# Kernel tuning notes

Hardware: AMD Instinct MI355X
Metric: run time of the kernel (lower is better)

Reference implementation:

```python
import jax, jax.numpy as jnp
import numpy as np

N_E = 8192
E_DIM = 256
BETA = 0.25
SIGMA = 0.1


def setup_inputs() -> dict:
    key = jax.random.key(0)
    kz, ke = jax.random.split(key)
    z = jax.random.normal(kz, (16, 256, 32, 32), dtype=jnp.float32)
    # torch init: uniform(-1/n_e, 1/n_e)
    emb = jax.random.uniform(ke, (N_E, E_DIM), minval=-1.0 / N_E, maxval=1.0 / N_E, dtype=jnp.float32)
    return {"z": z, "emb": emb}


def _vq_forward(z, emb, beta=BETA, sigma=SIGMA):
    b, c, h, w = z.shape  # c == e_dim
    z_bhwc = jnp.transpose(z, (0, 2, 3, 1))  # b h w c
    zf = z_bhwc.reshape(-1, c)  # [b*h*w, c]

    # d[i, n] = ||zf_i||^2 + ||e_n||^2 - 2 zf_i . e_n
    e2 = jnp.sum(emb ** 2, axis=1)  # [n_e]
    d = jnp.sum(zf ** 2, axis=1, keepdims=True) + e2 - 2.0 * (zf @ emb.T)  # [bhw, n_e]

    # codebook-codebook pairwise distances
    d1 = e2[:, None] + e2[None, :] - 2.0 * (emb @ emb.T)  # [n_e, n_e]
    # torch.kthvalue(d1, 2, 0): 2nd smallest along dim 0, per column
    min_dist = jnp.sort(d1, axis=0)[1]  # [n_e]
    total_min_distance = jnp.sum(min_dist)
    codebookvariance = jnp.std(min_dist, ddof=1)  # torch.std is unbiased

    min_encoding_indices = jnp.argmin(d, axis=1)  # [bhw]
    # d[range, argmin] == row-wise min
    distances = jnp.min(d, axis=1).reshape(b, h, w)
    # rbf: exp(-(d^2).mean(axis=1) / (2*sigma^2)) -> [b, w]
    distances = jnp.exp(-jnp.mean(distances ** 2, axis=1) / (2.0 * sigma ** 2))

    z_q = jnp.take(emb, min_encoding_indices, axis=0).reshape(b, h, w, c)

    sg = jax.lax.stop_gradient
    # legacy=True branch
    loss = (jnp.mean((sg(z_q) - z_bhwc) ** 2)
            + beta * jnp.mean((z_q - sg(z_bhwc)) ** 2)
            - total_min_distance)

    # straight-through estimator
    z_q = z_bhwc + sg(z_q - z_bhwc)
    z_q_bchw = jnp.transpose(z_q, (0, 3, 1, 2))  # b c h w (contiguous)
    # torch .view(b, h*w, e_dim) on contiguous bchw buffer: raw reshape
    z_flattened1 = z_q_bchw.reshape(b, h * w, c)

    return (z_q_bchw, loss, distances, min_encoding_indices,
            z_flattened1, codebookvariance, total_min_distance)


def reference(z, emb):
    return _vq_forward(z, emb)
```

## Files before the change

kernel.cpp:

```cpp
#include <hip/hip_runtime.h>
#include <stdint.h>

#define N_E   8192
#define EDIM  256
#define NB    16
#define HH    32
#define WW    32
#define HW    1024
#define NI    16384
#define NELEM 4194304

#define O_ZQ   0
#define O_LOSS 4194304
#define O_DIST 4194305
#define O_IDX  4194817
#define O_ZFL  4211201
#define O_CBV  8405505
#define O_TMD  8405506

#define WS_PMIN 0
#define WS_IDX  131072
#define WS_DMIN 196608
#define WS_E2   262144
#define WS_Z2   294912
#define WS_MSE  360448
#define WS_D1P  360512

__device__ __forceinline__ int row8(int ty, int r) {
    return (r < 4) ? (ty * 4 + r) : (64 + ty * 4 + (r - 4));
}

__global__ void k_init(unsigned long long* __restrict__ pmin, double* __restrict__ mse) {
    int t = blockIdx.x * 256 + threadIdx.x;
    if (t < NI) pmin[t] = 0xFFFFFFFFFFFFFFFFull;
    if (t == 0) *mse = 0.0;
}

__global__ void k_e2(const float* __restrict__ emb, float* __restrict__ e2) {
    int row  = blockIdx.x * 4 + (threadIdx.x >> 6);
    int lane = threadIdx.x & 63;
    float4 v = *reinterpret_cast<const float4*>(emb + (size_t)row * EDIM + lane * 4);
    float s = v.x * v.x + v.y * v.y + v.z * v.z + v.w * v.w;
    #pragma unroll
    for (int m = 32; m; m >>= 1) s += __shfl_xor(s, m);
    if (lane == 0) e2[row] = s;
}

__global__ void k_z2(const float* __restrict__ z, float* __restrict__ z2) {
    int i = blockIdx.x * 256 + threadIdx.x;
    int b = i >> 10, hw = i & 1023;
    const float* p = z + (size_t)b * EDIM * HW + hw;
    float s = 0.f;
    #pragma unroll 8
    for (int c = 0; c < EDIM; ++c) { float v = p[(size_t)c * HW]; s += v * v; }
    z2[i] = s;
}

__launch_bounds__(256)
__global__ void k_gemm_z(const float* __restrict__ z, const float* __restrict__ emb,
                         const float* __restrict__ z2, const float* __restrict__ e2,
                         unsigned long long* __restrict__ pmin) {
    __shared__ float a_lds[16][128];
    __shared__ float b_lds[16][128];
    const int t  = threadIdx.x;
    const int tx = t & 15, ty = t >> 4;
    const int i0 = blockIdx.x * 128;
    const int bb = i0 >> 10, hw0 = i0 & 1023;
    const int nbase = blockIdx.y * 1024;

    float minv[8], z2r[8];
    int   mini[8];
    #pragma unroll
    for (int r = 0; r < 8; ++r) {
        minv[r] = 3.4e38f; mini[r] = 0x7fffffff;
        z2r[r]  = z2[i0 + row8(ty, r)];
    }

    const int ak = t >> 4;
    const int ax = (t & 15) * 4;
    const float* zbase = z + (size_t)bb * EDIM * HW + hw0;
    const int bj = t >> 1;
    const int bc = (t & 1) * 8;

    for (int ns = 0; ns < 8; ++ns) {
        const int n0 = nbase + ns * 128;
        float acc[8][8];
        #pragma unroll
        for (int r = 0; r < 8; ++r)
            #pragma unroll
            for (int c = 0; c < 8; ++c) acc[r][c] = 0.f;

        for (int kc = 0; kc < 16; ++kc) {
            const int c0 = kc * 16;
            __syncthreads();
            *reinterpret_cast<float4*>(&a_lds[ak][ax]) =
                *reinterpret_cast<const float4*>(zbase + (size_t)(c0 + ak) * HW + ax);
            *reinterpret_cast<float4*>(&a_lds[ak][ax + 64]) =
                *reinterpret_cast<const float4*>(zbase + (size_t)(c0 + ak) * HW + ax + 64);
            {
                const float4 u = *reinterpret_cast<const float4*>(emb + (size_t)(n0 + bj) * EDIM + c0 + bc);
                const float4 v = *reinterpret_cast<const float4*>(emb + (size_t)(n0 + bj) * EDIM + c0 + bc + 4);
                b_lds[bc + 0][bj] = u.x; b_lds[bc + 1][bj] = u.y;
                b_lds[bc + 2][bj] = u.z; b_lds[bc + 3][bj] = u.w;
                b_lds[bc + 4][bj] = v.x; b_lds[bc + 5][bj] = v.y;
                b_lds[bc + 6][bj] = v.z; b_lds[bc + 7][bj] = v.w;
            }
            __syncthreads();
            #pragma unroll
            for (int k = 0; k < 16; ++k) {
                const float4 a0 = *reinterpret_cast<const float4*>(&a_lds[k][ty * 4]);
                const float4 a1 = *reinterpret_cast<const float4*>(&a_lds[k][64 + ty * 4]);
                const float4 b0 = *reinterpret_cast<const float4*>(&b_lds[k][tx * 4]);
                const float4 b1 = *reinterpret_cast<const float4*>(&b_lds[k][64 + tx * 4]);
                const float av[8] = {a0.x, a0.y, a0.z, a0.w, a1.x, a1.y, a1.z, a1.w};
                const float bv[8] = {b0.x, b0.y, b0.z, b0.w, b1.x, b1.y, b1.z, b1.w};
                #pragma unroll
                for (int r = 0; r < 8; ++r)
                    #pragma unroll
                    for (int c = 0; c < 8; ++c)
                        acc[r][c] = fmaf(av[r], bv[c], acc[r][c]);
            }
        }
        const float4 e0 = *reinterpret_cast<const float4*>(&e2[n0 + tx * 4]);
        const float4 e1 = *reinterpret_cast<const float4*>(&e2[n0 + 64 + tx * 4]);
        const float ev[8] = {e0.x, e0.y, e0.z, e0.w, e1.x, e1.y, e1.z, e1.w};
        #pragma unroll
        for (int r = 0; r < 8; ++r) {
            #pragma unroll
            for (int c = 0; c < 8; ++c) {
                const float d = (z2r[r] + ev[c]) - 2.0f * acc[r][c];
                const int   n = n0 + ((c < 4) ? (tx * 4 + c) : (64 + tx * 4 + (c - 4)));
                if (d < minv[r]) { minv[r] = d; mini[r] = n; }
            }
        }
    }
    #pragma unroll
    for (int r = 0; r < 8; ++r) {
        #pragma unroll
        for (int m = 1; m < 16; m <<= 1) {
            const float ov = __shfl_xor(minv[r], m);
            const int   oi = __shfl_xor(mini[r], m);
            if (ov < minv[r] || (ov == minv[r] && oi < mini[r])) { minv[r] = ov; mini[r] = oi; }
        }
        if (tx == 0) {
            const unsigned long long pk =
                ((unsigned long long)__float_as_uint(minv[r]) << 32) | (unsigned)mini[r];
            atomicMin(&pmin[i0 + row8(ty, r)], pk);
        }
    }
}

__launch_bounds__(256)
__global__ void k_gemm_d1(const float* __restrict__ emb, const float* __restrict__ e2,
                          float* __restrict__ d1p) {
    __shared__ float a_lds[16][128];
    __shared__ float b_lds[16][128];
    const int t  = threadIdx.x;
    const int tx = t & 15, ty = t >> 4;
    const int n0A   = blockIdx.x * 128;
    const int mbase = blockIdx.y * 1024;

    float v1[8], v2[8], e2a[8];
    #pragma unroll
    for (int r = 0; r < 8; ++r) { v1[r] = 3.4e38f; v2[r] = 3.4e38f; e2a[r] = e2[n0A + row8(ty, r)]; }

    const int aj = t >> 1;
    const int ac = (t & 1) * 8;

    for (int ms = 0; ms < 8; ++ms) {
        const int m0 = mbase + ms * 128;
        float acc[8][8];
        #pragma unroll
        for (int r = 0; r < 8; ++r)
            #pragma unroll
            for (int c = 0; c < 8; ++c) acc[r][c] = 0.f;

        for (int kc = 0; kc < 16; ++kc) {
            const int c0 = kc * 16;
            __syncthreads();
            {
                const float4 u = *reinterpret_cast<const float4*>(emb + (size_t)(n0A + aj) * EDIM + c0 + ac);
                const float4 v = *reinterpret_cast<const float4*>(emb + (size_t)(n0A + aj) * EDIM + c0 + ac + 4);
                a_lds[ac + 0][aj] = u.x; a_lds[ac + 1][aj] = u.y;
                a_lds[ac + 2][aj] = u.z; a_lds[ac + 3][aj] = u.w;
                a_lds[ac + 4][aj] = v.x; a_lds[ac + 5][aj] = v.y;
                a_lds[ac + 6][aj] = v.z; a_lds[ac + 7][aj] = v.w;
            }
            {
                const float4 u = *reinterpret_cast<const float4*>(emb + (size_t)(m0 + aj) * EDIM + c0 + ac);
                const float4 v = *reinterpret_cast<const float4*>(emb + (size_t)(m0 + aj) * EDIM + c0 + ac + 4);
                b_lds[ac + 0][aj] = u.x; b_lds[ac + 1][aj] = u.y;
                b_lds[ac + 2][aj] = u.z; b_lds[ac + 3][aj] = u.w;
                b_lds[ac + 4][aj] = v.x; b_lds[ac + 5][aj] = v.y;
                b_lds[ac + 6][aj] = v.z; b_lds[ac + 7][aj] = v.w;
            }
            __syncthreads();
            #pragma unroll
            for (int k = 0; k < 16; ++k) {
                const float4 a0 = *reinterpret_cast<const float4*>(&a_lds[k][ty * 4]);
                const float4 a1 = *reinterpret_cast<const float4*>(&a_lds[k][64 + ty * 4]);
                const float4 b0 = *reinterpret_cast<const float4*>(&b_lds[k][tx * 4]);
                const float4 b1 = *reinterpret_cast<const float4*>(&b_lds[k][64 + tx * 4]);
                const float av[8] = {a0.x, a0.y, a0.z, a0.w, a1.x, a1.y, a1.z, a1.w};
                const float bv[8] = {b0.x, b0.y, b0.z, b0.w, b1.x, b1.y, b1.z, b1.w};
                #pragma unroll
                for (int r = 0; r < 8; ++r)
                    #pragma unroll
                    for (int c = 0; c < 8; ++c)
                        acc[r][c] = fmaf(av[r], bv[c], acc[r][c]);
            }
        }
        const float4 e0 = *reinterpret_cast<const float4*>(&e2[m0 + tx * 4]);
        const float4 e1 = *reinterpret_cast<const float4*>(&e2[m0 + 64 + tx * 4]);
        const float eb[8] = {e0.x, e0.y, e0.z, e0.w, e1.x, e1.y, e1.z, e1.w};
        #pragma unroll
        for (int r = 0; r < 8; ++r) {
            #pragma unroll
            for (int c = 0; c < 8; ++c) {
                const float d = (eb[c] + e2a[r]) - 2.0f * acc[r][c];
                if (d < v1[r]) { v2[r] = v1[r]; v1[r] = d; }
                else if (d < v2[r]) { v2[r] = d; }
            }
        }
    }
    #pragma unroll
    for (int r = 0; r < 8; ++r) {
        #pragma unroll
        for (int m = 1; m < 16; m <<= 1) {
            const float o1 = __shfl_xor(v1[r], m);
            const float o2 = __shfl_xor(v2[r], m);
            const float nv1 = fminf(v1[r], o1);
            const float nv2 = fminf(fmaxf(v1[r], o1), fminf(v2[r], o2));
            v1[r] = nv1; v2[r] = nv2;
        }
        if (tx == 0) {
            const int n = n0A + row8(ty, r);
            d1p[((size_t)blockIdx.y * N_E + n) * 2 + 0] = v1[r];
            d1p[((size_t)blockIdx.y * N_E + n) * 2 + 1] = v2[r];
        }
    }
}

__global__ void k_unpack(const unsigned long long* __restrict__ pmin,
                         int* __restrict__ idxi, float* __restrict__ dmin,
                         float* __restrict__ out_idx) {
    int i = blockIdx.x * 256 + threadIdx.x;
    unsigned long long p = pmin[i];
    int idx  = (int)(p & 0xFFFFFFFFull);
    idxi[i]  = idx;
    dmin[i]  = __uint_as_float((unsigned)(p >> 32));
    out_idx[i] = (float)idx;
}

__global__ void k_epilogue(const float* __restrict__ z, const float* __restrict__ emb,
                           const int* __restrict__ idxi,
                           float* __restrict__ out_zq, float* __restrict__ out_zfl,
                           double* __restrict__ mse) {
    const int j4 = blockIdx.x * 256 + threadIdx.x;
    const int j  = j4 * 4;
    const int b  = j >> 18;
    const int c  = (j >> 10) & 255;
    const int hw = j & 1023;
    const int ib = (b << 10) + hw;
    const float4 zv = *reinterpret_cast<const float4*>(z + j);
    const float q0 = emb[(size_t)idxi[ib + 0] * EDIM + c];
    const float q1 = emb[(size_t)idxi[ib + 1] * EDIM + c];
    const float q2 = emb[(size_t)idxi[ib + 2] * EDIM + c];
    const float q3 = emb[(size_t)idxi[ib + 3] * EDIM + c];
    const float d0 = q0 - zv.x, d1 = q1 - zv.y, d2 = q2 - zv.z, d3 = q3 - zv.w;
    const float4 st = {zv.x + d0, zv.y + d1, zv.z + d2, zv.w + d3};
    *reinterpret_cast<float4*>(out_zq + j) = st;
    out_zfl[j + 0] = st.x; out_zfl[j + 1] = st.y; out_zfl[j + 2] = st.z; out_zfl[j + 3] = st.w;

    double s = (double)(d0 * d0) + (double)(d1 * d1) + (double)(d2 * d2) + (double)(d3 * d3);
    #pragma unroll
    for (int m = 32; m; m >>= 1) s += __shfl_down(s, m);
    __shared__ double part[4];
    if ((threadIdx.x & 63) == 0) part[threadIdx.x >> 6] = s;
    __syncthreads();
    if (threadIdx.x == 0) atomicAdd(mse, part[0] + part[1] + part[2] + part[3]);
}

__global__ void k_distances(const float* __restrict__ dmin, float* __restrict__ out_d) {
    int t = threadIdx.x;
    int b = t >> 5, w = t & 31;
    float s = 0.f;
    #pragma unroll
    for (int h = 0; h < HH; ++h) {
        float d = dmin[(b << 10) + (h << 5) + w];
        s += d * d;
    }
    float mean = s * (1.0f / 32.0f);
    out_d[t] = expf(-mean / 0.02f);
}

__global__ void k_finalize(const float* __restrict__ d1p, const double* __restrict__ mse,
                           float* __restrict__ out) {
    const int t = threadIdx.x;
    double s = 0.0, ss = 0.0;
    for (int n = t; n < N_E; n += 256) {
        float v1 = 3.4e38f, v2 = 3.4e38f;
        #pragma unroll
        for (int sp = 0; sp < 8; ++sp) {
            const float a1 = d1p[((size_t)sp * N_E + n) * 2 + 0];
            const float a2 = d1p[((size_t)sp * N_E + n) * 2 + 1];
            const float n1 = fminf(v1, a1);
            const float n2 = fminf(fmaxf(v1, a1), fminf(v2, a2));
            v1 = n1; v2 = n2;
        }
        s  += (double)v2;
        ss += (double)v2 * (double)v2;
    }
    #pragma unroll
    for (int m = 32; m; m >>= 1) { s += __shfl_down(s, m); ss += __shfl_down(ss, m); }
    __shared__ double rs[4], rss[4];
    if ((t & 63) == 0) { rs[t >> 6] = s; rss[t >> 6] = ss; }
    __syncthreads();
    if (t == 0) {
        const double S  = rs[0] + rs[1] + rs[2] + rs[3];
        const double SS = rss[0] + rss[1] + rss[2] + rss[3];
        const float tmd = (float)S;
        double var = (SS - S * S / (double)N_E) / (double)(N_E - 1);
        if (var < 0.0) var = 0.0;
        const float cbv = (float)sqrt(var);
        const float m1  = (float)(*mse / (double)NELEM);
        const float lossf = m1 + 0.25f * m1 - tmd;
        out[O_LOSS] = lossf;
        out[O_CBV]  = cbv;
        out[O_TMD]  = tmd;
    }
}

extern "C" void kernel_launch(void* const* d_in, const int* in_sizes, int n_in,
                              void* d_out, int out_size, void* d_ws, size_t ws_size,
                              hipStream_t stream) {
    const float* z   = (const float*)d_in[0];
    const float* emb = (const float*)d_in[1];
    float* out = (float*)d_out;
    char*  ws  = (char*)d_ws;

    unsigned long long* pmin = (unsigned long long*)(ws + WS_PMIN);
    int*    idxi = (int*)   (ws + WS_IDX);
    float*  dmin = (float*) (ws + WS_DMIN);
    float*  e2   = (float*) (ws + WS_E2);
    float*  z2   = (float*) (ws + WS_Z2);
    double* mse  = (double*)(ws + WS_MSE);
    float*  d1p  = (float*) (ws + WS_D1P);

    k_init     <<<64,   256, 0, stream>>>(pmin, mse);
    k_e2       <<<2048, 256, 0, stream>>>(emb, e2);
    k_z2       <<<64,   256, 0, stream>>>(z, z2);
    k_gemm_z   <<<dim3(128, 8), 256, 0, stream>>>(z, emb, z2, e2, pmin);
    k_gemm_d1  <<<dim3(64, 8),  256, 0, stream>>>(emb, e2, d1p);
    k_unpack   <<<64,   256, 0, stream>>>(pmin, idxi, dmin, out + O_IDX);
    k_epilogue <<<4096, 256, 0, stream>>>(z, emb, idxi, out + O_ZQ, out + O_ZFL, mse);
    k_distances<<<1,    512, 0, stream>>>(dmin, out + O_DIST);
    k_finalize <<<1,    256, 0, stream>>>(d1p, mse, out);
}
```

Baseline: 1.384 ms.

## Use bf16 MFMA candidate search with fp32 rescoring for both distance GEMMs

Replaces the fp32 FMA tiled GEMMs for the z-codebook and codebook-codebook distances with bf16 MFMA kernels on pre-converted, pre-laid-out operands. Each pass stores only per-32-column-group minima. Groups within a fixed margin of the row minimum are then rescored exactly in fp32 to recover the argmin and the second-smallest distance. This moves the dominant matmul work onto matrix cores, at the cost of extra conversion, selection and rescoring kernels. Exactness relies on fixed error margins and a capped item list, which may break for inputs with different scales.

```diff
diff --git a/kernel.cpp b/kernel.cpp
--- a/kernel.cpp
+++ b/kernel.cpp
@@ -10,6 +10,10 @@
 #define NI    16384
 #define NELEM 4194304
 
+#define MARGIN    2.5e-4f
+#define MARGIN_D1 2e-8f
+#define ITEM_CAP  262144
+
 #define O_ZQ   0
 #define O_LOSS 4194304
 #define O_DIST 4194305
@@ -18,22 +22,33 @@
 #define O_CBV  8405505
 #define O_TMD  8405506
 
-#define WS_PMIN 0
-#define WS_IDX  131072
-#define WS_DMIN 196608
-#define WS_E2   262144
-#define WS_Z2   294912
-#define WS_MSE  360448
-#define WS_D1P  360512
-
-__device__ __forceinline__ int row8(int ty, int r) {
-    return (r < 4) ? (ty * 4 + r) : (64 + ty * 4 + (r - 4));
-}
-
-__global__ void k_init(unsigned long long* __restrict__ pmin, double* __restrict__ mse) {
+#define WS_PMIN  0
+#define WS_IDX   131072
+#define WS_DMIN  196608
+#define WS_E2    262144
+#define WS_Z2    294912
+#define WS_MSE   360448
+#define WS_CNT   360456
+#define WS_MIND  360512
+#define WS_ZA    1048576
+#define WS_EB    9437184
+#define WS_M     13631488
+#define WS_ITEMS 30408704
+
+typedef __attribute__((ext_vector_type(8))) short bf16x8;
+typedef __attribute__((ext_vector_type(4))) float f32x4;
+
+__device__ __forceinline__ short f2bf(float f) {
+    unsigned u = __float_as_uint(f);
+    u += 0x7fffu + ((u >> 16) & 1u);
+    return (short)(u >> 16);
+}
+
+__global__ void k_init(unsigned long long* __restrict__ pmin, double* __restrict__ mse,
+                       int* __restrict__ cnt) {
     int t = blockIdx.x * 256 + threadIdx.x;
     if (t < NI) pmin[t] = 0xFFFFFFFFFFFFFFFFull;
-    if (t == 0) *mse = 0.0;
+    if (t == 0) { *mse = 0.0; *cnt = 0; }
 }
 
 __global__ void k_e2(const float* __restrict__ emb, float* __restrict__ e2) {
@@ -56,189 +71,252 @@
     z2[i] = s;
 }
 
-__launch_bounds__(256)
-__global__ void k_gemm_z(const float* __restrict__ z, const float* __restrict__ emb,
-                         const float* __restrict__ z2, const float* __restrict__ e2,
-                         unsigned long long* __restrict__ pmin) {
-    __shared__ float a_lds[16][128];
-    __shared__ float b_lds[16][128];
+__global__ void k_convert_z(const float* __restrict__ z, bf16x8* __restrict__ zA) {
+    __shared__ float lds[64][65];
+    const int t   = threadIdx.x;
+    const int hw0 = blockIdx.x * 64;
+    const int c0  = blockIdx.y * 64;
+    const int b   = blockIdx.z;
+    #pragma unroll
+    for (int cc = 0; cc < 4; ++cc) {
+        const int cl = cc * 16 + (t >> 4);
+        const float4 v = *reinterpret_cast<const float4*>(
+            z + ((size_t)(b * 256 + c0 + cl) << 10) + hw0 + (t & 15) * 4);
+        lds[cl][(t & 15) * 4 + 0] = v.x; lds[cl][(t & 15) * 4 + 1] = v.y;
+        lds[cl][(t & 15) * 4 + 2] = v.z; lds[cl][(t & 15) * 4 + 3] = v.w;
+    }
+    __syncthreads();
+    const int hl = t & 63;
+    const int i  = b * 1024 + hw0 + hl;
+    const int ig = i >> 4, r = i & 15;
+    #pragma unroll
+    for (int half = 0; half < 2; ++half) {
+        const int kqi = (t >> 6) + half * 4;
+        const int kq  = (c0 >> 3) + kqi;
+        bf16x8 o;
+        #pragma unroll
+        for (int j = 0; j < 8; ++j) o[j] = f2bf(lds[kqi * 8 + j][hl]);
+        zA[(ig * 32 + kq) * 16 + r] = o;
+    }
+}
+
+__global__ void k_convert_e(const float* __restrict__ emb, bf16x8* __restrict__ eB) {
     const int t  = threadIdx.x;
-    const int tx = t & 15, ty = t >> 4;
-    const int i0 = blockIdx.x * 128;
-    const int bb = i0 >> 10, hw0 = i0 & 1023;
-    const int nbase = blockIdx.y * 1024;
-
-    float minv[8], z2r[8];
-    int   mini[8];
-    #pragma unroll
-    for (int r = 0; r < 8; ++r) {
-        minv[r] = 3.4e38f; mini[r] = 0x7fffffff;
-        z2r[r]  = z2[i0 + row8(ty, r)];
-    }
-
-    const int ak = t >> 4;
-    const int ax = (t & 15) * 4;
-    const float* zbase = z + (size_t)bb * EDIM * HW + hw0;
-    const int bj = t >> 1;
-    const int bc = (t & 1) * 8;
+    const int kq = t & 31;
+    const int n  = blockIdx.x * 8 + (t >> 5);
+    const float4 u = *reinterpret_cast<const float4*>(emb + (size_t)n * EDIM + kq * 8);
+    const float4 v = *reinterpret_cast<const float4*>(emb + (size_t)n * EDIM + kq * 8 + 4);
+    bf16x8 o;
+    o[0] = f2bf(u.x); o[1] = f2bf(u.y); o[2] = f2bf(u.z); o[3] = f2bf(u.w);
+    o[4] = f2bf(v.x); o[5] = f2bf(v.y); o[6] = f2bf(v.z); o[7] = f2bf(v.w);
+    eB[((n >> 4) * 32 + kq) * 16 + (n & 15)] = o;
+}
+
+__launch_bounds__(256, 2)
+__global__ void k_cand(const bf16x8* __restrict__ zA, const bf16x8* __restrict__ eB,
+                       const float* __restrict__ e2, float* __restrict__ m) {
+    const int t = threadIdx.x;
+    const int w = t >> 6, l = t & 63;
+    const int lo16 = l & 15, hi4 = l >> 4;
+    const int iblk = blockIdx.x, chunk = blockIdx.y;
+    const int ig0 = (iblk * 128 + w * 32) >> 4;
+
+    bf16x8 a[2][8];
+    #pragma unroll
+    for (int ig = 0; ig < 2; ++ig)
+        #pragma unroll
+        for (int st = 0; st < 8; ++st)
+            a[ig][st] = zA[((ig0 + ig) * 32 + st * 4 + hi4) * 16 + lo16];
 
     for (int ns = 0; ns < 8; ++ns) {
-        const int n0 = nbase + ns * 128;
-        float acc[8][8];
-        #pragma unroll
-        for (int r = 0; r < 8; ++r)
-            #pragma unroll
-            for (int c = 0; c < 8; ++c) acc[r][c] = 0.f;
-
-        for (int kc = 0; kc < 16; ++kc) {
-            const int c0 = kc * 16;
-            __syncthreads();
-            *reinterpret_cast<float4*>(&a_lds[ak][ax]) =
-                *reinterpret_cast<const float4*>(zbase + (size_t)(c0 + ak) * HW + ax);
-            *reinterpret_cast<float4*>(&a_lds[ak][ax + 64]) =
-                *reinterpret_cast<const float4*>(zbase + (size_t)(c0 + ak) * HW + ax + 64);
-            {
-                const float4 u = *reinterpret_cast<const float4*>(emb + (size_t)(n0 + bj) * EDIM + c0 + bc);
-                const float4 v = *reinterpret_cast<const float4*>(emb + (size_t)(n0 + bj) * EDIM + c0 + bc + 4);
-                b_lds[bc + 0][bj] = u.x; b_lds[bc + 1][bj] = u.y;
-                b_lds[bc + 2][bj] = u.z; b_lds[bc + 3][bj] = u.w;
-                b_lds[bc + 4][bj] = v.x; b_lds[bc + 5][bj] = v.y;
-                b_lds[bc + 6][bj] = v.z; b_lds[bc + 7][bj] = v.w;
+        const int n0 = chunk * 1024 + ns * 128;
+        f32x4 acc[2][8];
+        #pragma unroll
+        for (int ig = 0; ig < 2; ++ig)
+            #pragma unroll
+            for (int cg = 0; cg < 8; ++cg) acc[ig][cg] = (f32x4){0.f, 0.f, 0.f, 0.f};
+        float e2v[8];
+        #pragma unroll
+        for (int cg = 0; cg < 8; ++cg) e2v[cg] = e2[n0 + cg * 16 + lo16];
+
+        #pragma unroll
+        for (int st = 0; st < 8; ++st) {
+            #pragma unroll
+            for (int cg = 0; cg < 8; ++cg) {
+                const bf16x8 b = eB[(((n0 >> 4) + cg) * 32 + st * 4 + hi4) * 16 + lo16];
+                acc[0][cg] = __builtin_amdgcn_mfma_f32_16x16x32_bf16(a[0][st], b, acc[0][cg], 0, 0, 0);
+                acc[1][cg] = __builtin_amdgcn_mfma_f32_16x16x32_bf16(a[1][st], b, acc[1][cg], 0, 0, 0);
             }
-            __syncthreads();
-            #pragma unroll
-            for (int k = 0; k < 16; ++k) {
-                const float4 a0 = *reinterpret_cast<const float4*>(&a_lds[k][ty * 4]);
-                const float4 a1 = *reinterpret_cast<const float4*>(&a_lds[k][64 + ty * 4]);
-                const float4 b0 = *reinterpret_cast<const float4*>(&b_lds[k][tx * 4]);
-                const float4 b1 = *reinterpret_cast<const float4*>(&b_lds[k][64 + tx * 4]);
-                const float av[8] = {a0.x, a0.y, a0.z, a0.w, a1.x, a1.y, a1.z, a1.w};
-                const float bv[8] = {b0.x, b0.y, b0.z, b0.w, b1.x, b1.y, b1.z, b1.w};
+        }
+        #pragma unroll
+        for (int ig = 0; ig < 2; ++ig) {
+            #pragma unroll
+            for (int reg = 0; reg < 4; ++reg) {
+                const int row = iblk * 128 + w * 32 + ig * 16 + hi4 * 4 + reg;
                 #pragma unroll
-                for (int r = 0; r < 8; ++r)
-                    #pragma unroll
-                    for (int c = 0; c < 8; ++c)
-                        acc[r][c] = fmaf(av[r], bv[c], acc[r][c]);
+                for (int gp = 0; gp < 4; ++gp) {
+                    float v = fminf(fmaf(-2.f, acc[ig][2 * gp][reg],     e2v[2 * gp]),
+                                    fmaf(-2.f, acc[ig][2 * gp + 1][reg], e2v[2 * gp + 1]));
+                    v = fminf(v, __shfl_xor(v, 1));
+                    v = fminf(v, __shfl_xor(v, 2));
+                    v = fminf(v, __shfl_xor(v, 4));
+                    v = fminf(v, __shfl_xor(v, 8));
+                    if (lo16 == gp) m[row * 256 + chunk * 32 + ns * 4 + gp] = v;
+                }
             }
         }
-        const float4 e0 = *reinterpret_cast<const float4*>(&e2[n0 + tx * 4]);
-        const float4 e1 = *reinterpret_cast<const float4*>(&e2[n0 + 64 + tx * 4]);
-        const float ev[8] = {e0.x, e0.y, e0.z, e0.w, e1.x, e1.y, e1.z, e1.w};
-        #pragma unroll
-        for (int r = 0; r < 8; ++r) {
-            #pragma unroll
-            for (int c = 0; c < 8; ++c) {
-                const float d = (z2r[r] + ev[c]) - 2.0f * acc[r][c];
-                const int   n = n0 + ((c < 4) ? (tx * 4 + c) : (64 + tx * 4 + (c - 4)));
-                if (d < minv[r]) { minv[r] = d; mini[r] = n; }
+    }
+}
+
+__launch_bounds__(256, 2)
+__global__ void k_cand_d1(const bf16x8* __restrict__ eB, const float* __restrict__ e2,
+                          float* __restrict__ md1) {
+    const int t = threadIdx.x;
+    const int w = t >> 6, l = t & 63;
+    const int lo16 = l & 15, hi4 = l >> 4;
+    const int iblk = blockIdx.x, chunk = blockIdx.y;
+    const int ig0 = (iblk * 128 + w * 32) >> 4;
+
+    bf16x8 a[2][8];
+    #pragma unroll
+    for (int ig = 0; ig < 2; ++ig)
+        #pragma unroll
+        for (int st = 0; st < 8; ++st)
+            a[ig][st] = eB[((ig0 + ig) * 32 + st * 4 + hi4) * 16 + lo16];
+
+    for (int ns = 0; ns < 8; ++ns) {
+        const int n0 = chunk * 1024 + ns * 128;
+        f32x4 acc[2][8];
+        #pragma unroll
+        for (int ig = 0; ig < 2; ++ig)
+            #pragma unroll
+            for (int cg = 0; cg < 8; ++cg) acc[ig][cg] = (f32x4){0.f, 0.f, 0.f, 0.f};
+        float e2v[8];
+        #pragma unroll
+        for (int cg = 0; cg < 8; ++cg) e2v[cg] = e2[n0 + cg * 16 + lo16];
+
+        #pragma unroll
+        for (int st = 0; st < 8; ++st) {
+            #pragma unroll
+            for (int cg = 0; cg < 8; ++cg) {
+                const bf16x8 b = eB[(((n0 >> 4) + cg) * 32 + st * 4 + hi4) * 16 + lo16];
+                acc[0][cg] = __builtin_amdgcn_mfma_f32_16x16x32_bf16(a[0][st], b, acc[0][cg], 0, 0, 0);
+                acc[1][cg] = __builtin_amdgcn_mfma_f32_16x16x32_bf16(a[1][st], b, acc[1][cg], 0, 0, 0);
             }
         }
-    }
-    #pragma unroll
-    for (int r = 0; r < 8; ++r) {
-        #pragma unroll
-        for (int m = 1; m < 16; m <<= 1) {
-            const float ov = __shfl_xor(minv[r], m);
-            const int   oi = __shfl_xor(mini[r], m);
-            if (ov < minv[r] || (ov == minv[r] && oi < mini[r])) { minv[r] = ov; mini[r] = oi; }
-        }
-        if (tx == 0) {
-            const unsigned long long pk =
-                ((unsigned long long)__float_as_uint(minv[r]) << 32) | (unsigned)mini[r];
-            atomicMin(&pmin[i0 + row8(ty, r)], pk);
-        }
-    }
-}
-
-__launch_bounds__(256)
-__global__ void k_gemm_d1(const float* __restrict__ emb, const float* __restrict__ e2,
-                          float* __restrict__ d1p) {
-    __shared__ float a_lds[16][128];
-    __shared__ float b_lds[16][128];
-    const int t  = threadIdx.x;
-    const int tx = t & 15, ty = t >> 4;
-    const int n0A   = blockIdx.x * 128;
-    const int mbase = blockIdx.y * 1024;
-
-    float v1[8], v2[8], e2a[8];
-    #pragma unroll
-    for (int r = 0; r < 8; ++r) { v1[r] = 3.4e38f; v2[r] = 3.4e38f; e2a[r] = e2[n0A + row8(ty, r)]; }
-
-    const int aj = t >> 1;
-    const int ac = (t & 1) * 8;
-
-    for (int ms = 0; ms < 8; ++ms) {
-        const int m0 = mbase + ms * 128;
-        float acc[8][8];
-        #pragma unroll
-        for (int r = 0; r < 8; ++r)
-            #pragma unroll
-            for (int c = 0; c < 8; ++c) acc[r][c] = 0.f;
-
-        for (int kc = 0; kc < 16; ++kc) {
-            const int c0 = kc * 16;
-            __syncthreads();
-            {
-                const float4 u = *reinterpret_cast<const float4*>(emb + (size_t)(n0A + aj) * EDIM + c0 + ac);
-                const float4 v = *reinterpret_cast<const float4*>(emb + (size_t)(n0A + aj) * EDIM + c0 + ac + 4);
-                a_lds[ac + 0][aj] = u.x; a_lds[ac + 1][aj] = u.y;
-                a_lds[ac + 2][aj] = u.z; a_lds[ac + 3][aj] = u.w;
-                a_lds[ac + 4][aj] = v.x; a_lds[ac + 5][aj] = v.y;
-                a_lds[ac + 6][aj] = v.z; a_lds[ac + 7][aj] = v.w;
+        #pragma unroll
+        for (int ig = 0; ig < 2; ++ig) {
+            #pragma unroll
+            for (int reg = 0; reg < 4; ++reg) {
+                const int row = iblk * 128 + w * 32 + ig * 16 + hi4 * 4 + reg;
+                #pragma unroll
+                for (int gp = 0; gp < 4; ++gp) {
+                    float v = fminf(fmaf(-2.f, acc[ig][2 * gp][reg],     e2v[2 * gp]),
+                                    fmaf(-2.f, acc[ig][2 * gp + 1][reg], e2v[2 * gp + 1]));
+                    v = fminf(v, __shfl_xor(v, 1));
+                    v = fminf(v, __shfl_xor(v, 2));
+                    v = fminf(v, __shfl_xor(v, 4));
+                    v = fminf(v, __shfl_xor(v, 8));
+                    if (lo16 == gp) md1[row * 256 + chunk * 32 + ns * 4 + gp] = v;
+                }
             }
-            {
-                const float4 u = *reinterpret_cast<const float4*>(emb + (size_t)(m0 + aj) * EDIM + c0 + ac);
-                const float4 v = *reinterpret_cast<const float4*>(emb + (size_t)(m0 + aj) * EDIM + c0 + ac + 4);
-                b_lds[ac + 0][aj] = u.x; b_lds[ac + 1][aj] = u.y;
-                b_lds[ac + 2][aj] = u.z; b_lds[ac + 3][aj] = u.w;
-                b_lds[ac + 4][aj] = v.x; b_lds[ac + 5][aj] = v.y;
-                b_lds[ac + 6][aj] = v.z; b_lds[ac + 7][aj] = v.w;
-            }
-            __syncthreads();
-            #pragma unroll
-            for (int k = 0; k < 16; ++k) {
-                const float4 a0 = *reinterpret_cast<const float4*>(&a_lds[k][ty * 4]);
-                const float4 a1 = *reinterpret_cast<const float4*>(&a_lds[k][64 + ty * 4]);
-                const float4 b0 = *reinterpret_cast<const float4*>(&b_lds[k][tx * 4]);
-                const float4 b1 = *reinterpret_cast<const float4*>(&b_lds[k][64 + tx * 4]);
-                const float av[8] = {a0.x, a0.y, a0.z, a0.w, a1.x, a1.y, a1.z, a1.w};
-                const float bv[8] = {b0.x, b0.y, b0.z, b0.w, b1.x, b1.y, b1.z, b1.w};
-                #pragma unroll
-                for (int r = 0; r < 8; ++r)
-                    #pragma unroll
-                    for (int c = 0; c < 8; ++c)
-                        acc[r][c] = fmaf(av[r], bv[c], acc[r][c]);
-            }
-        }
-        const float4 e0 = *reinterpret_cast<const float4*>(&e2[m0 + tx * 4]);
-        const float4 e1 = *reinterpret_cast<const float4*>(&e2[m0 + 64 + tx * 4]);
-        const float eb[8] = {e0.x, e0.y, e0.z, e0.w, e1.x, e1.y, e1.z, e1.w};
-        #pragma unroll
-        for (int r = 0; r < 8; ++r) {
-            #pragma unroll
-            for (int c = 0; c < 8; ++c) {
-                const float d = (eb[c] + e2a[r]) - 2.0f * acc[r][c];
-                if (d < v1[r]) { v2[r] = v1[r]; v1[r] = d; }
-                else if (d < v2[r]) { v2[r] = d; }
-            }
-        }
-    }
-    #pragma unroll
-    for (int r = 0; r < 8; ++r) {
-        #pragma unroll
-        for (int m = 1; m < 16; m <<= 1) {
-            const float o1 = __shfl_xor(v1[r], m);
-            const float o2 = __shfl_xor(v2[r], m);
-            const float nv1 = fminf(v1[r], o1);
-            const float nv2 = fminf(fmaxf(v1[r], o1), fminf(v2[r], o2));
-            v1[r] = nv1; v2[r] = nv2;
-        }
-        if (tx == 0) {
-            const int n = n0A + row8(ty, r);
-            d1p[((size_t)blockIdx.y * N_E + n) * 2 + 0] = v1[r];
-            d1p[((size_t)blockIdx.y * N_E + n) * 2 + 1] = v2[r];
-        }
-    }
+        }
+    }
+}
+
+__global__ void k_select(const float* __restrict__ m, int* __restrict__ cnt,
+                         unsigned* __restrict__ items) {
+    const int t = threadIdx.x;
+    const int row = blockIdx.x * 4 + (t >> 6);
+    const int l = t & 63;
+    const float4 mv = reinterpret_cast<const float4*>(m + (size_t)row * 256)[l];
+    float v = fminf(fminf(mv.x, mv.y), fminf(mv.z, mv.w));
+    #pragma unroll
+    for (int o = 32; o; o >>= 1) v = fminf(v, __shfl_xor(v, o));
+    const float thr = v + MARGIN;
+    if (mv.x <= thr) { int p = atomicAdd(cnt, 1); if (p < ITEM_CAP) items[p] = (row << 8) | (l * 4 + 0); }
+    if (mv.y <= thr) { int p = atomicAdd(cnt, 1); if (p < ITEM_CAP) items[p] = (row << 8) | (l * 4 + 1); }
+    if (mv.z <= thr) { int p = atomicAdd(cnt, 1); if (p < ITEM_CAP) items[p] = (row << 8) | (l * 4 + 2); }
+    if (mv.w <= thr) { int p = atomicAdd(cnt, 1); if (p < ITEM_CAP) items[p] = (row << 8) | (l * 4 + 3); }
+}
+
+__global__ void k_rescore(const float* __restrict__ z, const float* __restrict__ emb,
+                          const float* __restrict__ z2, const float* __restrict__ e2,
+                          const int* __restrict__ cnt, const unsigned* __restrict__ items,
+                          unsigned long long* __restrict__ pmin) {
+    const int t = threadIdx.x;
+    const int l = t & 63;
+    const int wid = blockIdx.x * 4 + (t >> 6);
+    int n_items = *cnt; if (n_items > ITEM_CAP) n_items = ITEM_CAP;
+    for (int it = wid; it < n_items; it += 16384) {
+        const unsigned item = items[it];
+        const int row = item >> 8, g = item & 255;
+        const int n = g * 32 + (l & 31);
+        const int half = l >> 5;
+        const float* zp = z + ((size_t)(row >> 10) << 18) + (row & 1023) + (size_t)(half * 128) * HW;
+        const float* ep = emb + (size_t)n * EDIM + half * 128;
+        float acc = 0.f;
+        #pragma unroll 8
+        for (int c = 0; c < 128; ++c) acc = fmaf(zp[(size_t)c * HW], ep[c], acc);
+        acc += __shfl_xor(acc, 32);
+        const float t0 = z2[row] + e2[n];
+        const float d  = fmaf(-2.f, acc, t0);
+        unsigned long long pk = ((unsigned long long)__float_as_uint(d) << 32) | (unsigned)n;
+        #pragma unroll
+        for (int o = 1; o < 64; o <<= 1) {
+            const unsigned long long op = __shfl_xor(pk, o);
+            if (op < pk) pk = op;
+        }
+        if (l == 0) atomicMin(&pmin[row], pk);
+    }
+}
+
+__global__ void k_d1_final(const float* __restrict__ emb, const float* __restrict__ e2,
+                           const float* __restrict__ md1, float* __restrict__ mind) {
+    const int t = threadIdx.x, l = t & 63;
+    const int n = blockIdx.x * 4 + (t >> 6);
+    const float4 mv = reinterpret_cast<const float4*>(md1 + (size_t)n * 256)[l];
+    const float lo1 = fminf(mv.x, mv.y), hi1 = fmaxf(mv.x, mv.y);
+    const float lo2 = fminf(mv.z, mv.w), hi2 = fmaxf(mv.z, mv.w);
+    float a1 = fminf(lo1, lo2);
+    float a2 = fminf(fmaxf(lo1, lo2), fminf(hi1, hi2));
+    #pragma unroll
+    for (int o = 1; o < 64; o <<= 1) {
+        const float o1 = __shfl_xor(a1, o), o2 = __shfl_xor(a2, o);
+        const float n1 = fminf(a1, o1);
+        const float n2 = fminf(fmaxf(a1, o1), fminf(a2, o2));
+        a1 = n1; a2 = n2;
+    }
+    const float thr = a2 + MARGIN_D1;
+    const float e2n = e2[n];
+    const float* np = emb + (size_t)n * EDIM;
+    float b1 = 3.4e38f, b2 = 3.4e38f;
+    const float slot[4] = {mv.x, mv.y, mv.z, mv.w};
+    #pragma unroll
+    for (int s = 0; s < 4; ++s) {
+        unsigned long long mask = __ballot(slot[s] <= thr);
+        while (mask) {
+            const int src = __builtin_ctzll(mask); mask &= mask - 1;
+            const int g = src * 4 + s;
+            const int mm = g * 32 + (l & 31);
+            const float* ep = emb + (size_t)mm * EDIM;
+            float acc = 0.f;
+            #pragma unroll 8
+            for (int c = 0; c < EDIM; ++c) acc = fmaf(ep[c], np[c], acc);
+            float dv = (e2[mm] + e2n) - 2.0f * acc;
+            if (l >= 32) dv = 3.4e38f;
+            if (dv < b1) { b2 = b1; b1 = dv; }
+            else if (dv < b2) { b2 = dv; }
+        }
+    }
+    #pragma unroll
+    for (int o = 1; o < 64; o <<= 1) {
+        const float o1 = __shfl_xor(b1, o), o2 = __shfl_xor(b2, o);
+        const float n1 = fminf(b1, o1);
+        const float n2 = fminf(fmaxf(b1, o1), fminf(b2, o2));
+        b1 = n1; b2 = n2;
+    }
+    if (l == 0) mind[n] = b2;
 }
 
 __global__ void k_unpack(const unsigned long long* __restrict__ pmin,
@@ -294,22 +372,13 @@
     out_d[t] = expf(-mean / 0.02f);
 }
 
-__global__ void k_finalize(const float* __restrict__ d1p, const double* __restrict__ mse,
+__global__ void k_finalize(const float* __restrict__ mind, const double* __restrict__ mse,
                            float* __restrict__ out) {
     const int t = threadIdx.x;
     double s = 0.0, ss = 0.0;
     for (int n = t; n < N_E; n += 256) {
-        float v1 = 3.4e38f, v2 = 3.4e38f;
-        #pragma unroll
-        for (int sp = 0; sp < 8; ++sp) {
-            const float a1 = d1p[((size_t)sp * N_E + n) * 2 + 0];
-            const float a2 = d1p[((size_t)sp * N_E + n) * 2 + 1];
-            const float n1 = fminf(v1, a1);
-            const float n2 = fminf(fmaxf(v1, a1), fminf(v2, a2));
-            v1 = n1; v2 = n2;
-        }
-        s  += (double)v2;
-        ss += (double)v2 * (double)v2;
+        const double v = (double)mind[n];
+        s += v; ss += v * v;
     }
     #pragma unroll
     for (int m = 32; m; m >>= 1) { s += __shfl_down(s, m); ss += __shfl_down(ss, m); }
@@ -340,20 +409,30 @@
     char*  ws  = (char*)d_ws;
 
     unsigned long long* pmin = (unsigned long long*)(ws + WS_PMIN);
-    int*    idxi = (int*)   (ws + WS_IDX);
-    float*  dmin = (float*) (ws + WS_DMIN);
-    float*  e2   = (float*) (ws + WS_E2);
-    float*  z2   = (float*) (ws + WS_Z2);
-    double* mse  = (double*)(ws + WS_MSE);
-    float*  d1p  = (float*) (ws + WS_D1P);
-
-    k_init     <<<64,   256, 0, stream>>>(pmin, mse);
+    int*      idxi  = (int*)    (ws + WS_IDX);
+    float*    dmin  = (float*)  (ws + WS_DMIN);
+    float*    e2    = (float*)  (ws + WS_E2);
+    float*    z2    = (float*)  (ws + WS_Z2);
+    double*   mse   = (double*) (ws + WS_MSE);
+    int*      cnt   = (int*)    (ws + WS_CNT);
+    float*    mind  = (float*)  (ws + WS_MIND);
+    bf16x8*   zA    = (bf16x8*) (ws + WS_ZA);
+    bf16x8*   eB    = (bf16x8*) (ws + WS_EB);
+    float*    marr  = (float*)  (ws + WS_M);
+    unsigned* items = (unsigned*)(ws + WS_ITEMS);
+
+    k_init     <<<64,   256, 0, stream>>>(pmin, mse, cnt);
     k_e2       <<<2048, 256, 0, stream>>>(emb, e2);
     k_z2       <<<64,   256, 0, stream>>>(z, z2);
-    k_gemm_z   <<<dim3(128, 8), 256, 0, stream>>>(z, emb, z2, e2, pmin);
-    k_gemm_d1  <<<dim3(64, 8),  256, 0, stream>>>(emb, e2, d1p);
+    k_convert_z<<<dim3(16, 4, 16), 256, 0, stream>>>(z, zA);
+    k_convert_e<<<1024, 256, 0, stream>>>(emb, eB);
+    k_cand     <<<dim3(128, 8), 256, 0, stream>>>(zA, eB, e2, marr);
+    k_select   <<<4096, 256, 0, stream>>>(marr, cnt, items);
+    k_rescore  <<<4096, 256, 0, stream>>>(z, emb, z2, e2, cnt, items, pmin);
+    k_cand_d1  <<<dim3(64, 8), 256, 0, stream>>>(eB, e2, marr);
+    k_d1_final <<<2048, 256, 0, stream>>>(emb, e2, marr, mind);
     k_unpack   <<<64,   256, 0, stream>>>(pmin, idxi, dmin, out + O_IDX);
     k_epilogue <<<4096, 256, 0, stream>>>(z, emb, idxi, out + O_ZQ, out + O_ZFL, mse);
     k_distances<<<1,    512, 0, stream>>>(dmin, out + O_DIST);
-    k_finalize <<<1,    256, 0, stream>>>(d1p, mse, out);
-}
+    k_finalize <<<1,    256, 0, stream>>>(mind, mse, out);
+}
```

New measurement: 1.165 ms. 1.19x faster.
